# Kernel optimization log

Hardware: AMD Instinct MI355X
Metric: run time of the kernel (lower is better)

Reference implementation:

```python
import jax, jax.numpy as jnp
import numpy as np

L, N = 200, 256  # event_list_length, num_nodes


def setup_inputs() -> dict:
    key = jax.random.key(0)
    ks = jax.random.split(key, 7)
    time = jax.random.uniform(ks[0], (2,), dtype=jnp.float32)
    event_list = jax.random.normal(ks[1], (L + 1, N, N), dtype=jnp.float32)
    u_begin = jax.random.uniform(ks[2], (N, N, 3), dtype=jnp.float32)
    # xavier-ish scales for params
    a = jax.random.normal(ks[3], (L, N, N, 3), dtype=jnp.float32) * 0.05
    w = jax.random.normal(ks[4], (L, N, 1, N), dtype=jnp.float32) * 0.05
    liner_w = jax.random.normal(ks[5], (N, 3), dtype=jnp.float32) * 0.5
    liner_b = jax.random.normal(ks[6], (N,), dtype=jnp.float32) * 0.1
    return {"time": time, "event_list": event_list, "u_begin": u_begin,
            "a": a, "w": w, "liner_w": liner_w, "liner_b": liner_b,
            "batch_size": 2}


def reference(time, event_list, u_begin, a, w, liner_w, liner_b, batch_size):
    # event_list[:-1]; consumed in pairs (start, start+1) with batch_size == 2
    T = event_list.shape[0] - 1
    S = T // batch_size                      # number of scan steps
    n = event_list.shape[1]
    e2 = event_list[:T].reshape(S, 2, n, n)          # [S,2,N,N]
    a2 = a[:T].reshape(S, 2, n, n, 3)                # [S,2,N,N,3]
    w2 = w[:T, :, 0, :].reshape(S, 2, n, n)          # [S,2,N,N] (squeeze the 1-dim)
    t0, t1 = time[0], time[1]                        # original always uses time[0], time[1]

    def step(u, xs):
        ep, ap, wp = xs                              # [2,N,N], [2,N,N,3], [2,N,N]
        # per-node scalar dot: w[start][node] @ event_begin[k][node]
        dot0 = jnp.einsum('nk,nk->n', wp[0], ep[0])  # [N]
        dot1 = jnp.einsum('nk,nk->n', wp[1], ep[1])
        # math.exp in the original returns a Python float -> constant w.r.t. autograd
        f0 = jax.lax.stop_gradient(jnp.exp(-dot0 * t0))[:, None, None]
        f1 = jax.lax.stop_gradient(jnp.exp(-dot1 * t1))[:, None, None]
        lamda = u + ap[0] * f0 + ap[1] * f1          # [N,N,3]
        temp = jax.nn.softmax(lamda, axis=-1)        # softmax over the 3-dim (dim=1 of [N,3] per node)
        # per-node Linear(3,1): temp[node] @ W_node^T + b_node -> [N,N]
        out = jnp.einsum('nmc,nc->nm', temp, liner_w) + liner_b[:, None]
        # state update was .detach().cpu().numpy() -> stop_gradient
        return jax.lax.stop_gradient(temp), out

    _, outs = jax.lax.scan(step, u_begin, (e2, a2, w2))
    return outs                                      # [S, N, N] == [T/2, N, N]
```

## Files before the change

kernel.cpp:

```cpp
#include <hip/hip_runtime.h>


#define NN   256
#define TT   200
#define SS   100
#define DD   10
#define NG   (50 / DD)

__global__ __launch_bounds__(256) void f_kernel(
    const float* __restrict__ timep,
    const float* __restrict__ ev,
    const float* __restrict__ w,
    float* __restrict__ fws)
{
    const int tid  = threadIdx.x;
    const int lane = tid & 63;
    const int row  = blockIdx.x * 4 + (tid >> 6);
    const int t    = row >> 8;
    const int n    = row & 255;

    const size_t off = (size_t)t * (NN * NN) + (size_t)n * NN;
    const float4 wv  = ((const float4*)(w  + off))[lane];
    const float4 evv = ((const float4*)(ev + off))[lane];

    float d = wv.x * evv.x;
    d = fmaf(wv.y, evv.y, d);
    d = fmaf(wv.z, evv.z, d);
    d = fmaf(wv.w, evv.w, d);
#pragma unroll
    for (int off2 = 1; off2 < 64; off2 <<= 1)
        d += __shfl_xor(d, off2, 64);

    if (lane == 0) {
        const float tsel = (t & 1) ? timep[1] : timep[0];
        fws[n * TT + t] = __expf(-d * tsel);
    }
}

__global__ __launch_bounds__(256, 4) void scan_kernel(
    const float* __restrict__ fws,
    const float* __restrict__ ub,
    const float* __restrict__ a,
    const float* __restrict__ lw,
    const float* __restrict__ lb,
    float* __restrict__ out)
{
    __shared__ float fs[TT];

    const int n    = blockIdx.x;
    const int qtr  = blockIdx.y;
    const int tid  = threadIdx.x;
    const int sub  = tid & 3;
    const int par  = sub >> 1;
    const int chain = qtr * 64 + (tid >> 2);

    if (tid < TT) fs[tid] = fws[n * TT + tid];

    const size_t TS    = (size_t)NN * NN * 3;
    const size_t cbase = (size_t)n * (NN * 3) + (size_t)chain * 3;

    float u0 = ub[cbase + 0];
    float u1 = ub[cbase + 1];
    float u2 = ub[cbase + 2];
    const float w0 = lw[n * 3 + 0];
    const float w1 = lw[n * 3 + 1];
    const float w2 = lw[n * 3 + 2];
    const float bb = lb[n];

    __syncthreads();

    const float* pf = a + (size_t)sub * TS + cbase;
    float rg[DD][3];
#pragma unroll
    for (int j = 0; j < DD; ++j) {
        rg[j][0] = pf[0];
        rg[j][1] = pf[1];
        rg[j][2] = pf[2];
        pf += 4 * TS;
    }

    float* op = out + (size_t)n * NN + chain;
    const bool sel = (par == 0);
    const bool st  = (sub == 0);

    for (int g = 0; g < NG; ++g) {
        const int kb = g * DD;
#pragma unroll
        for (int j = 0; j < DD; ++j) {
            const int k = kb + j;
            const float ff = fs[4 * k + sub];
            float v0 = rg[j][0] * ff;
            float v1 = rg[j][1] * ff;
            float v2 = rg[j][2] * ff;
            if (g != NG - 1) {
                rg[j][0] = pf[0];
                rg[j][1] = pf[1];
                rg[j][2] = pf[2];
                pf += 4 * TS;
            }
            float vv0 = v0 + __shfl_xor(v0, 1, 64);
            float vv1 = v1 + __shfl_xor(v1, 1, 64);
            float vv2 = v2 + __shfl_xor(v2, 1, 64);
            float b0 = __shfl_xor(vv0, 2, 64);
            float b1 = __shfl_xor(vv1, 2, 64);
            float b2 = __shfl_xor(vv2, 2, 64);
            {
                float l0 = u0 + (sel ? vv0 : b0);
                float l1 = u1 + (sel ? vv1 : b1);
                float l2 = u2 + (sel ? vv2 : b2);
                float mx  = fmaxf(l0, fmaxf(l1, l2));
                float e0  = __expf(l0 - mx);
                float e1  = __expf(l1 - mx);
                float e2  = __expf(l2 - mx);
                float inv = __builtin_amdgcn_rcpf(e0 + e1 + e2);
                u0 = e0 * inv;
                u1 = e1 * inv;
                u2 = e2 * inv;
                if (st) {
                    __builtin_nontemporal_store(
                        fmaf(u0, w0, fmaf(u1, w1, fmaf(u2, w2, bb))),
                        op + (size_t)(2 * k) * (NN * NN));
                }
            }
            {
                float l0 = u0 + (sel ? b0 : vv0);
                float l1 = u1 + (sel ? b1 : vv1);
                float l2 = u2 + (sel ? b2 : vv2);
                float mx  = fmaxf(l0, fmaxf(l1, l2));
                float e0  = __expf(l0 - mx);
                float e1  = __expf(l1 - mx);
                float e2  = __expf(l2 - mx);
                float inv = __builtin_amdgcn_rcpf(e0 + e1 + e2);
                u0 = e0 * inv;
                u1 = e1 * inv;
                u2 = e2 * inv;
                if (st) {
                    __builtin_nontemporal_store(
                        fmaf(u0, w0, fmaf(u1, w1, fmaf(u2, w2, bb))),
                        op + (size_t)(2 * k + 1) * (NN * NN));
                }
            }
        }
    }
}

extern "C" void kernel_launch(void* const* d_in, const int* in_sizes, int n_in,
                              void* d_out, int out_size, void* d_ws, size_t ws_size,
                              hipStream_t stream) {
    const float* timep = (const float*)d_in[0];
    const float* ev    = (const float*)d_in[1];
    const float* ub    = (const float*)d_in[2];
    const float* a     = (const float*)d_in[3];
    const float* w     = (const float*)d_in[4];
    const float* lw    = (const float*)d_in[5];
    const float* lb    = (const float*)d_in[6];
    float* out = (float*)d_out;
    float* fws = (float*)d_ws;

    f_kernel<<<(TT * NN) / 4, 256, 0, stream>>>(timep, ev, w, fws);
    scan_kernel<<<dim3(NN, 4), 256, 0, stream>>>(fws, ub, a, lw, lb, out);
}
```

Before: 316.1 us.

## Stage a-tensor through LDS ring with async global_load_lds, one chain per thread

Replaces the per-thread register prefetch of `a` (four lanes per chain, combined with shuffles) with a 6-deep LDS ring buffer. Whole waves fill it using global_load_lds, synchronised by explicit vmcnt waits and barriers. Each thread now owns one chain and reads its three coefficients for both time substeps from LDS, so the shuffles are gone. The grid shrinks from 1024 to 256 blocks. The goal is coalesced async streaming and overlap of memory with the serial softmax chain, at the cost of fewer blocks, block-wide barriers every step, and hand-tuned vmcnt counts that must match exactly.

Measured after the change: 308.0 us. 2.6% less time.

```diff
diff --git a/kernel.cpp b/kernel.cpp
--- a/kernel.cpp
+++ b/kernel.cpp
@@ -1,11 +1,10 @@
 #include <hip/hip_runtime.h>
 
 
-#define NN   256
-#define TT   200
-#define SS   100
-#define DD   10
-#define NG   (50 / DD)
+#define NN    256
+#define TT    200
+#define SS    100
+#define DRING 6
 
 __global__ __launch_bounds__(256) void f_kernel(
     const float* __restrict__ timep,
@@ -28,8 +27,7 @@
     d = fmaf(wv.z, evv.z, d);
     d = fmaf(wv.w, evv.w, d);
 #pragma unroll
-    for (int off2 = 1; off2 < 64; off2 <<= 1)
-        d += __shfl_xor(d, off2, 64);
+    for (int o = 1; o < 64; o <<= 1) d += __shfl_xor(d, o, 64);
 
     if (lane == 0) {
         const float tsel = (t & 1) ? timep[1] : timep[0];
@@ -37,7 +35,7 @@
     }
 }
 
-__global__ __launch_bounds__(256, 4) void scan_kernel(
+__global__ __launch_bounds__(256) void scan_kernel(
     const float* __restrict__ fws,
     const float* __restrict__ ub,
     const float* __restrict__ a,
@@ -45,103 +43,97 @@
     const float* __restrict__ lb,
     float* __restrict__ out)
 {
-    __shared__ float fs[TT];
+    __shared__ float stg[DRING][4][768];
+    __shared__ float fsl[TT];
 
     const int n    = blockIdx.x;
-    const int qtr  = blockIdx.y;
     const int tid  = threadIdx.x;
-    const int sub  = tid & 3;
-    const int par  = sub >> 1;
-    const int chain = qtr * 64 + (tid >> 2);
+    const int lane = tid & 63;
+    const int wv   = tid >> 6;
 
-    if (tid < TT) fs[tid] = fws[n * TT + tid];
+    if (tid < TT) fsl[tid] = fws[n * TT + tid];
 
-    const size_t TS    = (size_t)NN * NN * 3;
-    const size_t cbase = (size_t)n * (NN * 3) + (size_t)chain * 3;
-
-    float u0 = ub[cbase + 0];
-    float u1 = ub[cbase + 1];
-    float u2 = ub[cbase + 2];
+    const size_t cb = (size_t)n * (NN * 3) + (size_t)tid * 3;
+    float u0 = ub[cb + 0], u1 = ub[cb + 1], u2 = ub[cb + 2];
     const float w0 = lw[n * 3 + 0];
     const float w1 = lw[n * 3 + 1];
     const float w2 = lw[n * 3 + 2];
     const float bb = lb[n];
 
+    const int m3 = tid * 3;
+    float* op = out + (size_t)n * NN + tid;
+
     __syncthreads();
 
-    const float* pf = a + (size_t)sub * TS + cbase;
-    float rg[DD][3];
-#pragma unroll
-    for (int j = 0; j < DD; ++j) {
-        rg[j][0] = pf[0];
-        rg[j][1] = pf[1];
-        rg[j][2] = pf[2];
-        pf += 4 * TS;
-    }
+    const float* abase = a + (size_t)n * (NN * 3) + (size_t)lane * 4;
 
-    float* op = out + (size_t)n * NN + chain;
-    const bool sel = (par == 0);
-    const bool st  = (sub == 0);
+#define STAGE(qq, bidx)                                                        \
+    do {                                                                       \
+        const float* gp_ = abase + (size_t)(4 * (qq) + wv) * ((size_t)NN * NN * 3); \
+        float* lp_ = &stg[bidx][wv][0];                                        \
+        __builtin_amdgcn_global_load_lds(                                      \
+            (const __attribute__((address_space(1))) void*)gp_,                \
+            (__attribute__((address_space(3))) void*)lp_, 16, 0, 0);           \
+        __builtin_amdgcn_global_load_lds(                                      \
+            (const __attribute__((address_space(1))) void*)(gp_ + 256),        \
+            (__attribute__((address_space(3))) void*)(lp_ + 256), 16, 0, 0);   \
+        __builtin_amdgcn_global_load_lds(                                      \
+            (const __attribute__((address_space(1))) void*)(gp_ + 512),        \
+            (__attribute__((address_space(3))) void*)(lp_ + 512), 16, 0, 0);   \
+    } while (0)
 
-    for (int g = 0; g < NG; ++g) {
-        const int kb = g * DD;
-#pragma unroll
-        for (int j = 0; j < DD; ++j) {
-            const int k = kb + j;
-            const float ff = fs[4 * k + sub];
-            float v0 = rg[j][0] * ff;
-            float v1 = rg[j][1] * ff;
-            float v2 = rg[j][2] * ff;
-            if (g != NG - 1) {
-                rg[j][0] = pf[0];
-                rg[j][1] = pf[1];
-                rg[j][2] = pf[2];
-                pf += 4 * TS;
-            }
-            float vv0 = v0 + __shfl_xor(v0, 1, 64);
-            float vv1 = v1 + __shfl_xor(v1, 1, 64);
-            float vv2 = v2 + __shfl_xor(v2, 1, 64);
-            float b0 = __shfl_xor(vv0, 2, 64);
-            float b1 = __shfl_xor(vv1, 2, 64);
-            float b2 = __shfl_xor(vv2, 2, 64);
-            {
-                float l0 = u0 + (sel ? vv0 : b0);
-                float l1 = u1 + (sel ? vv1 : b1);
-                float l2 = u2 + (sel ? vv2 : b2);
-                float mx  = fmaxf(l0, fmaxf(l1, l2));
-                float e0  = __expf(l0 - mx);
-                float e1  = __expf(l1 - mx);
-                float e2  = __expf(l2 - mx);
-                float inv = __builtin_amdgcn_rcpf(e0 + e1 + e2);
-                u0 = e0 * inv;
-                u1 = e1 * inv;
-                u2 = e2 * inv;
-                if (st) {
-                    __builtin_nontemporal_store(
-                        fmaf(u0, w0, fmaf(u1, w1, fmaf(u2, w2, bb))),
-                        op + (size_t)(2 * k) * (NN * NN));
-                }
-            }
-            {
-                float l0 = u0 + (sel ? b0 : vv0);
-                float l1 = u1 + (sel ? b1 : vv1);
-                float l2 = u2 + (sel ? b2 : vv2);
-                float mx  = fmaxf(l0, fmaxf(l1, l2));
-                float e0  = __expf(l0 - mx);
-                float e1  = __expf(l1 - mx);
-                float e2  = __expf(l2 - mx);
-                float inv = __builtin_amdgcn_rcpf(e0 + e1 + e2);
-                u0 = e0 * inv;
-                u1 = e1 * inv;
-                u2 = e2 * inv;
-                if (st) {
-                    __builtin_nontemporal_store(
-                        fmaf(u0, w0, fmaf(u1, w1, fmaf(u2, w2, bb))),
-                        op + (size_t)(2 * k + 1) * (NN * NN));
-                }
-            }
+    STAGE(0, 0); STAGE(1, 1); STAGE(2, 2); STAGE(3, 3); STAGE(4, 4);
+
+#define STEPX(BI, SA, SB, FA, FB, SOUT)                                        \
+    do {                                                                       \
+        float l0 = fmaf(stg[BI][SA][m3 + 0], FA, fmaf(stg[BI][SB][m3 + 0], FB, u0)); \
+        float l1 = fmaf(stg[BI][SA][m3 + 1], FA, fmaf(stg[BI][SB][m3 + 1], FB, u1)); \
+        float l2 = fmaf(stg[BI][SA][m3 + 2], FA, fmaf(stg[BI][SB][m3 + 2], FB, u2)); \
+        float mx = fmaxf(l0, fmaxf(l1, l2));                                   \
+        float e0 = __expf(l0 - mx), e1 = __expf(l1 - mx), e2 = __expf(l2 - mx);\
+        float iv = __builtin_amdgcn_rcpf(e0 + e1 + e2);                        \
+        u0 = e0 * iv; u1 = e1 * iv; u2 = e2 * iv;                              \
+        __builtin_nontemporal_store(fmaf(u0, w0, fmaf(u1, w1, fmaf(u2, w2, bb))), \
+                                    op + (size_t)(SOUT) * (NN * NN));          \
+    } while (0)
+
+#define PHASE(GG, VN, DOSTAGE, BI)                                             \
+    do {                                                                       \
+        asm volatile("s_waitcnt vmcnt(" #VN ")" ::: "memory");                 \
+        __builtin_amdgcn_s_barrier();                                          \
+        asm volatile("" ::: "memory");                                         \
+        if (DOSTAGE) {                                                         \
+            const int bs_ = (BI) ? (BI) - 1 : (DRING - 1);                     \
+            STAGE((GG) + DRING - 1, bs_);                                      \
+        }                                                                      \
+        asm volatile("" ::: "memory");                                         \
+        const float fa0 = fsl[4 * (GG) + 0], fb0 = fsl[4 * (GG) + 1];          \
+        STEPX(BI, 0, 1, fa0, fb0, 2 * (GG));                                   \
+        const float fa1 = fsl[4 * (GG) + 2], fb1 = fsl[4 * (GG) + 3];          \
+        STEPX(BI, 2, 3, fa1, fb1, 2 * (GG) + 1);                               \
+    } while (0)
+
+    PHASE(0, 12, 1, 0);
+    PHASE(1, 14, 1, 1);
+    PHASE(2, 16, 1, 2);
+    PHASE(3, 18, 1, 3);
+    PHASE(4, 20, 1, 4);
+    {
+        int b = 5;
+        for (int g = 5; g <= 44; ++g) {
+            PHASE(g, 22, 1, b);
+            b = (b == DRING - 1) ? 0 : b + 1;
         }
     }
+    PHASE(45, 22, 0, 3);
+    PHASE(46, 19, 0, 4);
+    PHASE(47, 16, 0, 5);
+    PHASE(48, 13, 0, 0);
+    PHASE(49, 10, 0, 1);
+
+#undef PHASE
+#undef STEPX
+#undef STAGE
 }
 
 extern "C" void kernel_launch(void* const* d_in, const int* in_sizes, int n_in,
@@ -158,5 +150,5 @@
     float* fws = (float*)d_ws;
 
     f_kernel<<<(TT * NN) / 4, 256, 0, stream>>>(timep, ev, w, fws);
-    scan_kernel<<<dim3(NN, 4), 256, 0, stream>>>(fws, ub, a, lw, lb, out);
+    scan_kernel<<<NN, 256, 0, stream>>>(fws, ub, a, lw, lb, out);
 }
```
